# Kernel optimization log

Measured on AMD Instinct MI355X. Metric: run time of the kernel, lower is better.

Reference implementation:

```python
import jax, jax.numpy as jnp
import numpy as np

B, S, D = 2, 2048, 768
H, STRIDE = 12, 8
HD = D // H  # 64


def setup_inputs() -> dict:
    key = jax.random.key(0)
    k0, k1, k2 = jax.random.split(key, 3)
    x = jax.random.normal(k0, (B, S, D), dtype=jnp.float32)
    qkv_w = jax.random.normal(k1, (3 * D, D), dtype=jnp.float32) * 0.02
    qkv_b = jnp.zeros((3 * D,), dtype=jnp.float32)
    out_w = jax.random.normal(k2, (D, D), dtype=jnp.float32) * 0.02
    out_b = jnp.zeros((D,), dtype=jnp.float32)
    return {"x": x, "qkv_w": qkv_w, "qkv_b": qkv_b, "out_w": out_w, "out_b": out_b}


def _stride_mask(S, stride, causal):
    i = jnp.arange(S)[:, None]
    j = jnp.arange(S)[None, :]
    strided = (j % stride == 0)
    if causal:
        strided = strided & (j <= i)
    # diagonal always attended; previous token attended for i > 0
    return strided | (j == i) | (j == i - 1)


def reference(x, qkv_w, qkv_b, out_w, out_b):
    Bx, Sx, Dx = x.shape
    qkv = x @ qkv_w.T + qkv_b                      # [B,S,3D]
    qkv = qkv.reshape(Bx, Sx, 3, H, HD)
    q, k, v = jnp.transpose(qkv, (2, 0, 3, 1, 4))  # each [B,H,S,HD]
    scale = HD ** -0.5
    attn = jnp.einsum('bhid,bhjd->bhij', q, k) * scale  # [B,H,S,S]
    mask = _stride_mask(Sx, STRIDE, True)          # [S,S] bool
    attn = jnp.where(mask[None, None], attn, -jnp.inf)
    a = jax.nn.softmax(attn, axis=-1)
    # every row has at least the diagonal unmasked, so no NaN rows;
    # nan_to_num kept for exact parity with the torch module
    a = jnp.nan_to_num(a, nan=0.0)
    out = jnp.einsum('bhij,bhjd->bhid', a, v)      # [B,H,S,HD]
    out = jnp.transpose(out, (0, 2, 1, 3)).reshape(Bx, Sx, Dx)
    return out @ out_w.T + out_b
```

## Files before the change

kernel.cpp:

```cpp
#include <hip/hip_runtime.h>
#include <hip/hip_bf16.h>
#include <stdint.h>

#define H_   12
#define S_   2048
#define D_   768
#define HD_  64
#define MS_  256

typedef __bf16 bf16_8 __attribute__((ext_vector_type(8)));
typedef float  f32_4  __attribute__((ext_vector_type(4)));

typedef __attribute__((address_space(1))) void* gas_ptr;
typedef __attribute__((address_space(3))) void* las_ptr;

__device__ __forceinline__ void g2l16(const void* g, void* l) {
  __builtin_amdgcn_global_load_lds((gas_ptr)g, (las_ptr)l, 16, 0, 0);
}

__device__ __forceinline__ f32_4 mfma16(bf16_8 a, bf16_8 b, f32_4 c) {
  return __builtin_amdgcn_mfma_f32_16x16x32_bf16(a, b, c, 0, 0, 0);
}

__device__ __forceinline__ bf16_8 ld8(const __hip_bfloat16* p) {
  return *reinterpret_cast<const bf16_8*>(p);
}

__global__ __launch_bounds__(256) void cvt3_f32_bf16(
    const float* __restrict__ a, const float* __restrict__ b,
    const float* __restrict__ c, __hip_bfloat16* __restrict__ out,
    int na4, int nb4) {
  const int t = blockIdx.x * 256 + threadIdx.x;
  float4 f;
  if (t < na4)            f = reinterpret_cast<const float4*>(a)[t];
  else if (t < na4 + nb4) f = reinterpret_cast<const float4*>(b)[t - na4];
  else                    f = reinterpret_cast<const float4*>(c)[t - na4 - nb4];
  union { __hip_bfloat16 h[4]; ushort4 u; } p;
  p.h[0] = __float2bfloat16(f.x);
  p.h[1] = __float2bfloat16(f.y);
  p.h[2] = __float2bfloat16(f.z);
  p.h[3] = __float2bfloat16(f.w);
  reinterpret_cast<ushort4*>(out)[t] = p.u;
}

template <int MODE, int BN>
__global__ __launch_bounds__(256, 2) void gemm_bt(
    const __hip_bfloat16* __restrict__ A, const __hip_bfloat16* __restrict__ B,
    const float* __restrict__ bias,
    __hip_bfloat16* __restrict__ O0, __hip_bfloat16* __restrict__ O1,
    __hip_bfloat16* __restrict__ O2, __hip_bfloat16* __restrict__ O3,
    float* __restrict__ OF, int M, int N, int K) {
  constexpr int NTJ = BN / 32;
  __shared__ __bf16 sA[128 * 32];
  __shared__ __bf16 sB[BN * 32];
  const int tid  = threadIdx.x;
  const int lane = tid & 63;
  const int wv   = tid >> 6;
  const int m0 = blockIdx.y * 128;
  const int n0 = blockIdx.x * BN;
  const int wr = (wv >> 1) * 64;
  const int wc = (wv & 1) * (BN / 2);

  f32_4 acc[4][NTJ] = {};

  const __hip_bfloat16* aS = A + (size_t)(m0 + (tid >> 2)) * K + ((tid & 3) << 3);
  const __hip_bfloat16* bS = B + (size_t)(n0 + (tid >> 2)) * K + ((tid & 3) << 3);
  const size_t half = (size_t)64 * K;
  __bf16* dA  = &sA[tid * 8];
  __bf16* dA2 = &sA[tid * 8 + 2048];
  __bf16* dB  = &sB[tid * 8];
  __bf16* dB2 = &sB[tid * 8 + 2048];

  const int fr = lane & 15;
  const int kq = (lane >> 4) << 3;

  for (int k0 = 0; k0 < K; k0 += 32) {
    g2l16(aS, dA);
    g2l16(aS + half, dA2);
    g2l16(bS, dB);
    if constexpr (BN == 128) g2l16(bS + half, dB2);
    aS += 32;
    bS += 32;
    __syncthreads();
    bf16_8 af[4], bfm[NTJ];
#pragma unroll
    for (int t = 0; t < 4; ++t)
      af[t] = *reinterpret_cast<const bf16_8*>(&sA[(wr + t * 16 + fr) * 32 + kq]);
#pragma unroll
    for (int t = 0; t < NTJ; ++t)
      bfm[t] = *reinterpret_cast<const bf16_8*>(&sB[(wc + t * 16 + fr) * 32 + kq]);
#pragma unroll
    for (int ti = 0; ti < 4; ++ti)
#pragma unroll
      for (int tj = 0; tj < NTJ; ++tj)
        acc[ti][tj] = mfma16(af[ti], bfm[tj], acc[ti][tj]);
    __syncthreads();
  }

  const int crow = (lane >> 4) << 2;
  const int ccol = lane & 15;
#pragma unroll
  for (int ti = 0; ti < 4; ++ti) {
    const int gmb = m0 + wr + ti * 16 + crow;
#pragma unroll
    for (int tj = 0; tj < NTJ; ++tj) {
      const int gn = n0 + wc + tj * 16 + ccol;
      const float bv = bias[gn];
      if (MODE == 0) {
        const int t   = gn / D_;
        const int rem = gn - t * D_;
        const int hh = rem >> 6, dd = rem & 63;
        if (t < 2) {
          __hip_bfloat16* dst = (t == 0) ? O0 : O1;
#pragma unroll
          for (int r = 0; r < 4; ++r) {
            const int gm = gmb + r;
            const int bb = gm >> 11, ss = gm & (S_ - 1);
            dst[(((size_t)(bb * H_ + hh) << 11) + ss) * HD_ + dd] =
                __float2bfloat16(acc[ti][tj][r] + bv);
          }
        } else {
          const int bb = gmb >> 11, ss = gmb & (S_ - 1);
          union { ushort4 u; __hip_bfloat16 h[4]; } pk;
#pragma unroll
          for (int r = 0; r < 4; ++r) pk.h[r] = __float2bfloat16(acc[ti][tj][r] + bv);
          const size_t rowb = ((size_t)(bb * H_ + hh) * HD_ + dd);
          *reinterpret_cast<ushort4*>(O2 + rowb * S_ + ss) = pk.u;
          if ((ss & 7) == 0) O3[rowb * MS_ + (ss >> 3)] = pk.h[0];
        }
      } else {
#pragma unroll
        for (int r = 0; r < 4; ++r)
          OF[(size_t)(gmb + r) * D_ + gn] = acc[ti][tj][r] + bv;
      }
    }
  }
}

__global__ __launch_bounds__(256) void attn_mfma(
    const __hip_bfloat16* __restrict__ Q, const __hip_bfloat16* __restrict__ Kb,
    const __hip_bfloat16* __restrict__ VT, const __hip_bfloat16* __restrict__ VsT,
    __hip_bfloat16* __restrict__ ctx) {
  __shared__ __bf16 pt[4][16 * 40];
  const int lane = threadIdx.x & 63;
  const int wv   = threadIdx.x >> 6;
  const int task = blockIdx.x * 4 + wv;
  const int bh   = task >> 7;
  const int i0   = (task & 127) << 4;
  const int lr   = lane & 15;
  const int quad = lane >> 4;
  const float SC  = 0.125f * 1.44269504088896340736f;

  const __hip_bfloat16* Kh  = Kb  + ((size_t)bh << 11) * HD_;
  const __hip_bfloat16* VTh = VT  + (size_t)bh * HD_ * S_;
  const __hip_bfloat16* Vsh = VsT + (size_t)bh * HD_ * MS_;
  __bf16* ptw = pt[wv];

  const __hip_bfloat16* qp = Q + (((size_t)bh << 11) + i0 + lr) * HD_ + quad * 8;
  const bf16_8 qf0 = ld8(qp);
  const bf16_8 qf1 = ld8(qp + 32);

  const __bf16 one = (__bf16)1.0f;
  const bf16_8 onesf = {one, one, one, one, one, one, one, one};

  f32_4 Lacc = {}, oacc[4];
#pragma unroll
  for (int ct = 0; ct < 4; ++ct) oacc[ct] = f32_4{0.f, 0.f, 0.f, 0.f};

  const int mmax = (i0 + 15) >> 3;
  const int nstr = (mmax >> 5) + 1;
  for (int c = 0; c <= nstr; ++c) {
    const bool strided = (c < nstr);
    const int  mb    = c << 5;
    const int  jbase = (i0 >= 8) ? (i0 - 8) : 0;

    bf16_8 kf[2][2], vf[4];
    if (strided) {
#pragma unroll
      for (int t = 0; t < 2; ++t) {
        const int m = mb + t * 16 + lr;
        const __hip_bfloat16* kp = Kh + ((size_t)m << 3) * HD_ + quad * 8;
        kf[t][0] = ld8(kp);
        kf[t][1] = ld8(kp + 32);
      }
#pragma unroll
      for (int ct = 0; ct < 4; ++ct)
        vf[ct] = ld8(Vsh + (size_t)(ct * 16 + lr) * MS_ + mb + quad * 8);
    } else {
#pragma unroll
      for (int t = 0; t < 2; ++t) {
        const int j  = jbase + t * 16 + lr;
        const int jr = (j < S_) ? j : (S_ - 1);
        const __hip_bfloat16* kp = Kh + (size_t)jr * HD_ + quad * 8;
        kf[t][0] = ld8(kp);
        kf[t][1] = ld8(kp + 32);
      }
      const int vs0 = jbase + quad * 8;
      const int vs  = (vs0 <= S_ - 8) ? vs0 : (S_ - 8);
#pragma unroll
      for (int ct = 0; ct < 4; ++ct)
        vf[ct] = ld8(VTh + (size_t)(ct * 16 + lr) * S_ + vs);
    }

    f32_4 s0 = {}, s1 = {};
    s0 = mfma16(qf0, kf[0][0], s0);
    s0 = mfma16(qf1, kf[0][1], s0);
    s1 = mfma16(qf0, kf[1][0], s1);
    s1 = mfma16(qf1, kf[1][1], s1);

#pragma unroll
    for (int r = 0; r < 4; ++r) {
      const int i = i0 + quad * 4 + r;
      bool v0, v1;
      if (strided) {
        v0 = ((mb + lr) << 3) <= i;
        v1 = ((mb + 16 + lr) << 3) <= i;
      } else {
        const int j0 = jbase + lr, j1 = jbase + 16 + lr;
        v0 = (j0 == i || j0 == i - 1) && (j0 & 7);
        v1 = (j1 == i || j1 == i - 1) && (j1 & 7);
      }
      s0[r] = v0 ? exp2f(fminf(s0[r] * SC, 63.f)) : 0.f;
      s1[r] = v1 ? exp2f(fminf(s1[r] * SC, 63.f)) : 0.f;
    }

#pragma unroll
    for (int r = 0; r < 4; ++r) {
      const int row = quad * 4 + r;
      ptw[row * 40 + lr]      = (__bf16)__float2bfloat16(s0[r]);
      ptw[row * 40 + 16 + lr] = (__bf16)__float2bfloat16(s1[r]);
    }
    const bf16_8 pf = *reinterpret_cast<const bf16_8*>(&ptw[lr * 40 + quad * 8]);

#pragma unroll
    for (int ct = 0; ct < 4; ++ct) oacc[ct] = mfma16(pf, vf[ct], oacc[ct]);
    Lacc = mfma16(pf, onesf, Lacc);
  }

  const int b = bh / H_;
  const int h = bh - b * H_;
  f32_4 inv;
#pragma unroll
  for (int r = 0; r < 4; ++r) inv[r] = 1.f / Lacc[r];
#pragma unroll
  for (int r = 0; r < 4; ++r) {
    const int i = i0 + quad * 4 + r;
    __hip_bfloat16* cp = ctx + ((size_t)(b * S_ + i)) * D_ + h * HD_ + lr;
#pragma unroll
    for (int ct = 0; ct < 4; ++ct)
      cp[ct * 16] = __float2bfloat16(oacc[ct][r] * inv[r]);
  }
}

extern "C" void kernel_launch(void* const* d_in, const int* in_sizes, int n_in,
                              void* d_out, int out_size, void* d_ws, size_t ws_size,
                              hipStream_t stream) {
  const float* x    = (const float*)d_in[0];
  const float* qkvw = (const float*)d_in[1];
  const float* qkvb = (const float*)d_in[2];
  const float* outw = (const float*)d_in[3];
  const float* outb = (const float*)d_in[4];
  float* out = (float*)d_out;

  const size_t NX  = (size_t)2 * S_ * D_;
  const size_t NW1 = (size_t)3 * D_ * D_;
  const size_t NW2 = (size_t)D_ * D_;
  const size_t NVS = (size_t)2 * H_ * HD_ * MS_;

  __hip_bfloat16* xb  = (__hip_bfloat16*)d_ws;
  __hip_bfloat16* w1b = xb + NX;
  __hip_bfloat16* w2b = w1b + NW1;
  __hip_bfloat16* q   = w2b + NW2;
  __hip_bfloat16* k   = q + NX;
  __hip_bfloat16* vt  = k + NX;
  __hip_bfloat16* vst = vt + NX;
  __hip_bfloat16* ctx = vst + NVS;

  const int na4 = (int)(NX / 4), nb4 = (int)(NW1 / 4), nc4 = (int)(NW2 / 4);
  cvt3_f32_bf16<<<dim3((na4 + nb4 + nc4) / 256), 256, 0, stream>>>(
      x, qkvw, outw, xb, na4, nb4);

  gemm_bt<0, 128><<<dim3(2304 / 128, 4096 / 128), 256, 0, stream>>>(
      xb, w1b, qkvb, q, k, vt, vst, nullptr, 4096, 2304, 768);

  attn_mfma<<<dim3(2 * H_ * S_ / 16 / 4), 256, 0, stream>>>(q, k, vt, vst, ctx);

  gemm_bt<1, 64><<<dim3(768 / 64, 4096 / 128), 256, 0, stream>>>(
      ctx, w2b, outb, nullptr, nullptr, nullptr, nullptr, out, 4096, 768, 768);
}
```

Before: 151.6 us.

## Fuse all four stages into one persistent cooperative kernel with grid syncs

Replaces the four separate launches (conversion, QKV GEMM, attention, output GEMM) with a single cooperative persistent kernel. The stages are separated by grid-wide barriers and each block loops over tiles or tasks. The goal is to remove launch gaps and tail effects between kernels. In exchange, the grid is capped at 512 blocks, blocks now walk work items serially, shared memory is sized for the larger GEMM tile, and the grid syncs with threadfences add their own cost.

```diff
diff --git a/kernel.cpp b/kernel.cpp
--- a/kernel.cpp
+++ b/kernel.cpp
@@ -1,6 +1,9 @@
 #include <hip/hip_runtime.h>
+#include <hip/hip_cooperative_groups.h>
 #include <hip/hip_bf16.h>
 #include <stdint.h>
+
+namespace cg = cooperative_groups;
 
 #define H_   12
 #define S_   2048
@@ -8,6 +11,11 @@
 #define HD_  64
 #define MS_  256
 
+constexpr int NXc  = 2 * S_ * D_;
+constexpr int NW1c = 3 * D_ * D_;
+constexpr int NW2c = D_ * D_;
+constexpr int NVSc = 2 * H_ * HD_ * MS_;
+
 typedef __bf16 bf16_8 __attribute__((ext_vector_type(8)));
 typedef float  f32_4  __attribute__((ext_vector_type(4)));
 
@@ -26,38 +34,34 @@
   return *reinterpret_cast<const bf16_8*>(p);
 }
 
-__global__ __launch_bounds__(256) void cvt3_f32_bf16(
-    const float* __restrict__ a, const float* __restrict__ b,
-    const float* __restrict__ c, __hip_bfloat16* __restrict__ out,
-    int na4, int nb4) {
-  const int t = blockIdx.x * 256 + threadIdx.x;
-  float4 f;
-  if (t < na4)            f = reinterpret_cast<const float4*>(a)[t];
-  else if (t < na4 + nb4) f = reinterpret_cast<const float4*>(b)[t - na4];
-  else                    f = reinterpret_cast<const float4*>(c)[t - na4 - nb4];
-  union { __hip_bfloat16 h[4]; ushort4 u; } p;
-  p.h[0] = __float2bfloat16(f.x);
-  p.h[1] = __float2bfloat16(f.y);
-  p.h[2] = __float2bfloat16(f.z);
-  p.h[3] = __float2bfloat16(f.w);
-  reinterpret_cast<ushort4*>(out)[t] = p.u;
+__device__ __forceinline__ void cvt_phase(
+    const float* x, const float* w1, const float* w2, __hip_bfloat16* dst) {
+  constexpr int na4 = NXc / 4, nb4 = NW1c / 4, nc4 = NW2c / 4;
+  const int T = gridDim.x * 256;
+  for (int t = blockIdx.x * 256 + threadIdx.x; t < na4 + nb4 + nc4; t += T) {
+    float4 f;
+    if (t < na4)            f = reinterpret_cast<const float4*>(x)[t];
+    else if (t < na4 + nb4) f = reinterpret_cast<const float4*>(w1)[t - na4];
+    else                    f = reinterpret_cast<const float4*>(w2)[t - na4 - nb4];
+    union { __hip_bfloat16 h[4]; ushort4 u; } p;
+    p.h[0] = __float2bfloat16(f.x);
+    p.h[1] = __float2bfloat16(f.y);
+    p.h[2] = __float2bfloat16(f.z);
+    p.h[3] = __float2bfloat16(f.w);
+    reinterpret_cast<ushort4*>(dst)[t] = p.u;
+  }
 }
 
 template <int MODE, int BN>
-__global__ __launch_bounds__(256, 2) void gemm_bt(
-    const __hip_bfloat16* __restrict__ A, const __hip_bfloat16* __restrict__ B,
-    const float* __restrict__ bias,
-    __hip_bfloat16* __restrict__ O0, __hip_bfloat16* __restrict__ O1,
-    __hip_bfloat16* __restrict__ O2, __hip_bfloat16* __restrict__ O3,
-    float* __restrict__ OF, int M, int N, int K) {
+__device__ __forceinline__ void gemm_tile(
+    const __hip_bfloat16* A, const __hip_bfloat16* B, const float* bias,
+    __hip_bfloat16* O0, __hip_bfloat16* O1, __hip_bfloat16* O2,
+    __hip_bfloat16* O3, float* OF, int m0, int n0, __bf16* sA, __bf16* sB) {
+  constexpr int K   = 768;
   constexpr int NTJ = BN / 32;
-  __shared__ __bf16 sA[128 * 32];
-  __shared__ __bf16 sB[BN * 32];
   const int tid  = threadIdx.x;
   const int lane = tid & 63;
   const int wv   = tid >> 6;
-  const int m0 = blockIdx.y * 128;
-  const int n0 = blockIdx.x * BN;
   const int wr = (wv >> 1) * 64;
   const int wc = (wv & 1) * (BN / 2);
 
@@ -66,10 +70,10 @@
   const __hip_bfloat16* aS = A + (size_t)(m0 + (tid >> 2)) * K + ((tid & 3) << 3);
   const __hip_bfloat16* bS = B + (size_t)(n0 + (tid >> 2)) * K + ((tid & 3) << 3);
   const size_t half = (size_t)64 * K;
-  __bf16* dA  = &sA[tid * 8];
-  __bf16* dA2 = &sA[tid * 8 + 2048];
-  __bf16* dB  = &sB[tid * 8];
-  __bf16* dB2 = &sB[tid * 8 + 2048];
+  __bf16* dA  = sA + tid * 8;
+  __bf16* dA2 = sA + tid * 8 + 2048;
+  __bf16* dB  = sB + tid * 8;
+  __bf16* dB2 = sB + tid * 8 + 2048;
 
   const int fr = lane & 15;
   const int kq = (lane >> 4) << 3;
@@ -85,10 +89,10 @@
     bf16_8 af[4], bfm[NTJ];
 #pragma unroll
     for (int t = 0; t < 4; ++t)
-      af[t] = *reinterpret_cast<const bf16_8*>(&sA[(wr + t * 16 + fr) * 32 + kq]);
+      af[t] = *reinterpret_cast<const bf16_8*>(sA + (wr + t * 16 + fr) * 32 + kq);
 #pragma unroll
     for (int t = 0; t < NTJ; ++t)
-      bfm[t] = *reinterpret_cast<const bf16_8*>(&sB[(wc + t * 16 + fr) * 32 + kq]);
+      bfm[t] = *reinterpret_cast<const bf16_8*>(sB + (wc + t * 16 + fr) * 32 + kq);
 #pragma unroll
     for (int ti = 0; ti < 4; ++ti)
 #pragma unroll
@@ -137,24 +141,20 @@
   }
 }
 
-__global__ __launch_bounds__(256) void attn_mfma(
-    const __hip_bfloat16* __restrict__ Q, const __hip_bfloat16* __restrict__ Kb,
-    const __hip_bfloat16* __restrict__ VT, const __hip_bfloat16* __restrict__ VsT,
-    __hip_bfloat16* __restrict__ ctx) {
-  __shared__ __bf16 pt[4][16 * 40];
+__device__ void attn_task(
+    const __hip_bfloat16* Q, const __hip_bfloat16* Kb,
+    const __hip_bfloat16* VT, const __hip_bfloat16* VsT,
+    __hip_bfloat16* ctx, int task, __bf16* ptw) {
   const int lane = threadIdx.x & 63;
-  const int wv   = threadIdx.x >> 6;
-  const int task = blockIdx.x * 4 + wv;
   const int bh   = task >> 7;
   const int i0   = (task & 127) << 4;
   const int lr   = lane & 15;
   const int quad = lane >> 4;
-  const float SC  = 0.125f * 1.44269504088896340736f;
+  const float SC = 0.125f * 1.44269504088896340736f;
 
   const __hip_bfloat16* Kh  = Kb  + ((size_t)bh << 11) * HD_;
   const __hip_bfloat16* VTh = VT  + (size_t)bh * HD_ * S_;
   const __hip_bfloat16* Vsh = VsT + (size_t)bh * HD_ * MS_;
-  __bf16* ptw = pt[wv];
 
   const __hip_bfloat16* qp = Q + (((size_t)bh << 11) + i0 + lr) * HD_ + quad * 8;
   const bf16_8 qf0 = ld8(qp);
@@ -230,7 +230,7 @@
       ptw[row * 40 + lr]      = (__bf16)__float2bfloat16(s0[r]);
       ptw[row * 40 + 16 + lr] = (__bf16)__float2bfloat16(s1[r]);
     }
-    const bf16_8 pf = *reinterpret_cast<const bf16_8*>(&ptw[lr * 40 + quad * 8]);
+    const bf16_8 pf = *reinterpret_cast<const bf16_8*>(ptw + lr * 40 + quad * 8);
 
 #pragma unroll
     for (int ct = 0; ct < 4; ++ct) oacc[ct] = mfma16(pf, vf[ct], oacc[ct]);
@@ -250,6 +250,47 @@
     for (int ct = 0; ct < 4; ++ct)
       cp[ct * 16] = __float2bfloat16(oacc[ct][r] * inv[r]);
   }
+}
+
+__global__ __launch_bounds__(256, 2) void mega(
+    const float* __restrict__ x, const float* __restrict__ qkvw,
+    const float* __restrict__ qkvb, const float* __restrict__ outw,
+    const float* __restrict__ outb, float* out, __hip_bfloat16* ws) {
+  __shared__ __bf16 sA[128 * 32];
+  __shared__ __bf16 sB[128 * 32];
+
+  __hip_bfloat16* xb  = ws;
+  __hip_bfloat16* w1b = xb + NXc;
+  __hip_bfloat16* w2b = w1b + NW1c;
+  __hip_bfloat16* q   = w2b + NW2c;
+  __hip_bfloat16* k   = q + NXc;
+  __hip_bfloat16* vt  = k + NXc;
+  __hip_bfloat16* vst = vt + NXc;
+  __hip_bfloat16* ctx = vst + NVSc;
+
+  cg::grid_group grid = cg::this_grid();
+
+  cvt_phase(x, qkvw, outw, xb);
+  __threadfence();
+  grid.sync();
+
+  for (int t = blockIdx.x; t < 576; t += gridDim.x)
+    gemm_tile<0, 128>(xb, w1b, qkvb, q, k, vt, vst, nullptr,
+                      (t / 18) * 128, (t % 18) * 128, sA, sB);
+  __threadfence();
+  grid.sync();
+
+  {
+    const int wv = threadIdx.x >> 6;
+    for (int bt = blockIdx.x; bt < 768; bt += gridDim.x)
+      attn_task(q, k, vt, vst, ctx, bt * 4 + wv, sA + wv * 640);
+  }
+  __threadfence();
+  grid.sync();
+
+  for (int t = blockIdx.x; t < 384; t += gridDim.x)
+    gemm_tile<1, 64>(ctx, w2b, outb, nullptr, nullptr, nullptr, nullptr, out,
+                     (t / 12) * 128, (t % 12) * 64, sA, sB);
 }
 
 extern "C" void kernel_launch(void* const* d_in, const int* in_sizes, int n_in,
@@ -261,30 +302,16 @@
   const float* outw = (const float*)d_in[3];
   const float* outb = (const float*)d_in[4];
   float* out = (float*)d_out;
-
-  const size_t NX  = (size_t)2 * S_ * D_;
-  const size_t NW1 = (size_t)3 * D_ * D_;
-  const size_t NW2 = (size_t)D_ * D_;
-  const size_t NVS = (size_t)2 * H_ * HD_ * MS_;
-
-  __hip_bfloat16* xb  = (__hip_bfloat16*)d_ws;
-  __hip_bfloat16* w1b = xb + NX;
-  __hip_bfloat16* w2b = w1b + NW1;
-  __hip_bfloat16* q   = w2b + NW2;
-  __hip_bfloat16* k   = q + NX;
-  __hip_bfloat16* vt  = k + NX;
-  __hip_bfloat16* vst = vt + NX;
-  __hip_bfloat16* ctx = vst + NVS;
-
-  const int na4 = (int)(NX / 4), nb4 = (int)(NW1 / 4), nc4 = (int)(NW2 / 4);
-  cvt3_f32_bf16<<<dim3((na4 + nb4 + nc4) / 256), 256, 0, stream>>>(
-      x, qkvw, outw, xb, na4, nb4);
-
-  gemm_bt<0, 128><<<dim3(2304 / 128, 4096 / 128), 256, 0, stream>>>(
-      xb, w1b, qkvb, q, k, vt, vst, nullptr, 4096, 2304, 768);
-
-  attn_mfma<<<dim3(2 * H_ * S_ / 16 / 4), 256, 0, stream>>>(q, k, vt, vst, ctx);
-
-  gemm_bt<1, 64><<<dim3(768 / 64, 4096 / 128), 256, 0, stream>>>(
-      ctx, w2b, outb, nullptr, nullptr, nullptr, nullptr, out, 4096, 768, 768);
-}
+  __hip_bfloat16* ws = (__hip_bfloat16*)d_ws;
+
+  int nb = 0;
+  if (hipOccupancyMaxActiveBlocksPerMultiprocessor(&nb, mega, 256, 0) != hipSuccess
+      || nb < 1)
+    nb = 1;
+  int gsz = nb * 256;
+  if (gsz > 512) gsz = 512;
+
+  void* args[] = {(void*)&x, (void*)&qkvw, (void*)&qkvb, (void*)&outw,
+                  (void*)&outb, (void*)&out, (void*)&ws};
+  hipLaunchCooperativeKernel(mega, dim3(gsz), dim3(256), args, 0, stream);
+}
```

New measurement: 366.1 us. +141.5%, slower.

## Compact strided K rows in QKV epilogue and double-buffer attention chunk loads

Applied to the files above, without the earlier changes.

The QKV GEMM epilogue now also writes every eighth K row into a compact per-head buffer, so the attention kernel reads strided keys contiguously instead of striding 8 rows apart. The attention loop is software-pipelined: the next chunk's K and V fragments are loaded into a second register set while the current chunk's MFMAs run, to hide global load latency. This costs extra registers and a small additional write in the GEMM epilogue.

```diff
diff --git a/kernel.cpp b/kernel.cpp
--- a/kernel.cpp
+++ b/kernel.cpp
@@ -49,7 +49,8 @@
     const float* __restrict__ bias,
     __hip_bfloat16* __restrict__ O0, __hip_bfloat16* __restrict__ O1,
     __hip_bfloat16* __restrict__ O2, __hip_bfloat16* __restrict__ O3,
-    float* __restrict__ OF, int M, int N, int K) {
+    __hip_bfloat16* __restrict__ O4, float* __restrict__ OF,
+    int M, int N, int K) {
   constexpr int NTJ = BN / 32;
   __shared__ __bf16 sA[128 * 32];
   __shared__ __bf16 sB[BN * 32];
@@ -116,8 +117,10 @@
           for (int r = 0; r < 4; ++r) {
             const int gm = gmb + r;
             const int bb = gm >> 11, ss = gm & (S_ - 1);
-            dst[(((size_t)(bb * H_ + hh) << 11) + ss) * HD_ + dd] =
-                __float2bfloat16(acc[ti][tj][r] + bv);
+            const __hip_bfloat16 hv = __float2bfloat16(acc[ti][tj][r] + bv);
+            dst[(((size_t)(bb * H_ + hh) << 11) + ss) * HD_ + dd] = hv;
+            if (t == 1 && r == 0 && (gmb & 7) == 0)
+              O4[(((size_t)(bb * H_ + hh)) * MS_ + (ss >> 3)) * HD_ + dd] = hv;
           }
         } else {
           const int bb = gmb >> 11, ss = gmb & (S_ - 1);
@@ -139,8 +142,8 @@
 
 __global__ __launch_bounds__(256) void attn_mfma(
     const __hip_bfloat16* __restrict__ Q, const __hip_bfloat16* __restrict__ Kb,
-    const __hip_bfloat16* __restrict__ VT, const __hip_bfloat16* __restrict__ VsT,
-    __hip_bfloat16* __restrict__ ctx) {
+    const __hip_bfloat16* __restrict__ Ks, const __hip_bfloat16* __restrict__ VT,
+    const __hip_bfloat16* __restrict__ VsT, __hip_bfloat16* __restrict__ ctx) {
   __shared__ __bf16 pt[4][16 * 40];
   const int lane = threadIdx.x & 63;
   const int wv   = threadIdx.x >> 6;
@@ -149,9 +152,10 @@
   const int i0   = (task & 127) << 4;
   const int lr   = lane & 15;
   const int quad = lane >> 4;
-  const float SC  = 0.125f * 1.44269504088896340736f;
+  const float SC = 0.125f * 1.44269504088896340736f;
 
   const __hip_bfloat16* Kh  = Kb  + ((size_t)bh << 11) * HD_;
+  const __hip_bfloat16* Ksh = Ks  + (size_t)bh * MS_ * HD_;
   const __hip_bfloat16* VTh = VT  + (size_t)bh * HD_ * S_;
   const __hip_bfloat16* Vsh = VsT + (size_t)bh * HD_ * MS_;
   __bf16* ptw = pt[wv];
@@ -167,19 +171,16 @@
 #pragma unroll
   for (int ct = 0; ct < 4; ++ct) oacc[ct] = f32_4{0.f, 0.f, 0.f, 0.f};
 
-  const int mmax = (i0 + 15) >> 3;
-  const int nstr = (mmax >> 5) + 1;
-  for (int c = 0; c <= nstr; ++c) {
-    const bool strided = (c < nstr);
-    const int  mb    = c << 5;
-    const int  jbase = (i0 >= 8) ? (i0 - 8) : 0;
-
-    bf16_8 kf[2][2], vf[4];
-    if (strided) {
+  const int mmax  = (i0 + 15) >> 3;
+  const int nstr  = (mmax >> 5) + 1;
+  const int jbase = (i0 >= 8) ? (i0 - 8) : 0;
+
+  auto load_chunk = [&](int c, bf16_8 (&kf)[2][2], bf16_8 (&vf)[4]) {
+    if (c < nstr) {
+      const int mb = c << 5;
 #pragma unroll
       for (int t = 0; t < 2; ++t) {
-        const int m = mb + t * 16 + lr;
-        const __hip_bfloat16* kp = Kh + ((size_t)m << 3) * HD_ + quad * 8;
+        const __hip_bfloat16* kp = Ksh + (size_t)(mb + t * 16 + lr) * HD_ + quad * 8;
         kf[t][0] = ld8(kp);
         kf[t][1] = ld8(kp + 32);
       }
@@ -201,6 +202,16 @@
       for (int ct = 0; ct < 4; ++ct)
         vf[ct] = ld8(VTh + (size_t)(ct * 16 + lr) * S_ + vs);
     }
+  };
+
+  bf16_8 kf[2][2], vf[4], kf2[2][2], vf2[4];
+  load_chunk(0, kf, vf);
+
+  for (int c = 0; c <= nstr; ++c) {
+    if (c < nstr) load_chunk(c + 1, kf2, vf2);
+
+    const bool strided = (c < nstr);
+    const int  mb      = c << 5;
 
     f32_4 s0 = {}, s1 = {};
     s0 = mfma16(qf0, kf[0][0], s0);
@@ -235,6 +246,13 @@
 #pragma unroll
     for (int ct = 0; ct < 4; ++ct) oacc[ct] = mfma16(pf, vf[ct], oacc[ct]);
     Lacc = mfma16(pf, onesf, Lacc);
+
+    if (c < nstr) {
+#pragma unroll
+      for (int t = 0; t < 2; ++t) { kf[t][0] = kf2[t][0]; kf[t][1] = kf2[t][1]; }
+#pragma unroll
+      for (int ct = 0; ct < 4; ++ct) vf[ct] = vf2[ct];
+    }
   }
 
   const int b = bh / H_;
@@ -274,17 +292,19 @@
   __hip_bfloat16* k   = q + NX;
   __hip_bfloat16* vt  = k + NX;
   __hip_bfloat16* vst = vt + NX;
-  __hip_bfloat16* ctx = vst + NVS;
+  __hip_bfloat16* ks  = vst + NVS;
+  __hip_bfloat16* ctx = ks + NVS;
 
   const int na4 = (int)(NX / 4), nb4 = (int)(NW1 / 4), nc4 = (int)(NW2 / 4);
   cvt3_f32_bf16<<<dim3((na4 + nb4 + nc4) / 256), 256, 0, stream>>>(
       x, qkvw, outw, xb, na4, nb4);
 
   gemm_bt<0, 128><<<dim3(2304 / 128, 4096 / 128), 256, 0, stream>>>(
-      xb, w1b, qkvb, q, k, vt, vst, nullptr, 4096, 2304, 768);
-
-  attn_mfma<<<dim3(2 * H_ * S_ / 16 / 4), 256, 0, stream>>>(q, k, vt, vst, ctx);
+      xb, w1b, qkvb, q, k, vt, vst, ks, nullptr, 4096, 2304, 768);
+
+  attn_mfma<<<dim3(2 * H_ * S_ / 16 / 4), 256, 0, stream>>>(q, k, ks, vt, vst, ctx);
 
   gemm_bt<1, 64><<<dim3(768 / 64, 4096 / 128), 256, 0, stream>>>(
-      ctx, w2b, outb, nullptr, nullptr, nullptr, nullptr, out, 4096, 768, 768);
-}
+      ctx, w2b, outb, nullptr, nullptr, nullptr, nullptr, nullptr,
+      out, 4096, 768, 768);
+}
```

Result: no change. 151.9 us (+0.2%).
